# Performance work log

Measured on AMD Instinct MI355X. Metric: run time of the kernel, lower is better.

## Reference

```python
import jax, jax.numpy as jnp
import numpy as np

N = 100000   # nodes
E = 1600000  # edges (node pairs)
D = 64       # msg_feature_len
H = 128      # hidden width of gate/message MLPs


def setup_inputs() -> dict:
    key = jax.random.key(0)
    ks = jax.random.split(key, 10)
    s = 0.05
    return {
        "node_weights": jax.random.uniform(ks[0], (N, 1), dtype=jnp.float32),
        "node_prev_features": jax.random.normal(ks[1], (N, D), dtype=jnp.float32),
        "self_idx": jax.random.randint(ks[2], (E,), 0, N),
        "neighbor_idx": jax.random.randint(ks[3], (E,), 0, N),
        "gw1": jax.random.normal(ks[4], (2 * D, H), dtype=jnp.float32) * s,
        "gb1": jnp.zeros((H,), jnp.float32),
        "gw2": jax.random.normal(ks[5], (H, 1), dtype=jnp.float32) * s,
        "gb2": jnp.zeros((1,), jnp.float32),
        "mw1": jax.random.normal(ks[6], (2 * D, H), dtype=jnp.float32) * s,
        "mb1": jnp.zeros((H,), jnp.float32),
        "mw2": jax.random.normal(ks[7], (H, D), dtype=jnp.float32) * s,
        "mb2": jnp.zeros((D,), jnp.float32),
        "pow_p": jax.random.normal(ks[8], (1,), dtype=jnp.float32),
    }


def reference(node_weights, node_prev_features, self_idx, neighbor_idx,
              gw1, gb1, gw2, gb2, mw1, mb1, mw2, mb2, pow_p):
    # gather + concat: message [E, 2D]
    msg = jnp.concatenate(
        [node_prev_features[self_idx], node_prev_features[neighbor_idx]], axis=1)
    w = node_weights[neighbor_idx]  # [E, 1]

    # gate MLP (Linear -> ReLU -> Linear): [E, 1]
    gate = jax.nn.relu(msg @ gw1 + gb1) @ gw2 + gb2
    # segment-softmax over edges grouped by self_idx, weighted by w**pow
    gmax = jax.ops.segment_max(gate, self_idx, num_segments=N)  # [N, 1]
    gate = (w ** pow_p) * jnp.exp(gate - gmax[self_idx])
    gsum = jax.ops.segment_sum(gate, self_idx, num_segments=N)  # [N, 1]
    gate = gate / (gsum[self_idx] + 1e-10)

    # message MLP: [E, D]
    x = jax.nn.relu(msg @ mw1 + mb1) @ mw2 + mb2

    # weighted scatter-sum back to nodes; single head -> mean is identity
    node_update = jax.ops.segment_sum(gate * x, self_idx, num_segments=N)
    return node_update + node_prev_features
```

## Files before the change

### kernel.cpp

```cpp
#include <hip/hip_runtime.h>
#include <hip/hip_bf16.h>

typedef __bf16 bf16x8 __attribute__((ext_vector_type(8)));
typedef float f32x4 __attribute__((ext_vector_type(4)));

#define WIN 64
#define TILE 112
#define CHUNK 7
#define LSTR 136
#define SCAN_BLK 1024
#define SENT 0x7f7f7f7f

__global__ void k_wconv(const float* __restrict__ gw1, const float* __restrict__ mw1,
                        const float* __restrict__ mw2,
                        __bf16* __restrict__ Bt, __bf16* __restrict__ mw2t,
                        int* __restrict__ hist, int* __restrict__ s_lo,
                        int* __restrict__ s_hi, int N, int NB)
{
    int i = blockIdx.x * 256 + threadIdx.x;
    if (i < 32768) {
        int c = i >> 6, k = i & 63;
        float v;
        if (c < 128)      v = gw1[k * 128 + c];
        else if (c < 256) v = gw1[(64 + k) * 128 + (c - 128)];
        else if (c < 384) v = mw1[k * 128 + (c - 256)];
        else              v = mw1[(64 + k) * 128 + (c - 384)];
        Bt[i] = (__bf16)v;
    } else if (i < 40960) {
        int j = i - 32768;
        int c = j >> 7, k = j & 127;
        mw2t[j] = (__bf16)mw2[k * 64 + c];
    }
    if (i < N) hist[i] = 0;
    if (i < NB) { s_lo[i] = SENT; s_hi[i] = 0; }
}

__global__ void __launch_bounds__(256, 4)
k_tab(const float* __restrict__ feat, const __bf16* __restrict__ Bt,
      const float* __restrict__ gb1, const float* __restrict__ mb1,
      const int* __restrict__ selfi, int* __restrict__ hist,
      __bf16* __restrict__ Tp, __bf16* __restrict__ Tq, int N, int E)
{
    for (int e = blockIdx.x * 256 + threadIdx.x; e < E; e += gridDim.x * 256)
        atomicAdd(&hist[selfi[e]], 1);

    const int tid = threadIdx.x;
    const int lane = tid & 63, wv = tid >> 6;
    const int la = lane & 15, kg = lane >> 4;
    const int r0 = blockIdx.x * 16;
    if (r0 >= N) return;

    bf16x8 a[2];
    #pragma unroll
    for (int kk = 0; kk < 2; ++kk) {
        const int rr = min(r0 + la, N - 1);
        const float* src = feat + (size_t)rr * 64 + kk * 32 + kg * 8;
        f32x4 f0 = *reinterpret_cast<const f32x4*>(src);
        f32x4 f1 = *reinterpret_cast<const f32x4*>(src + 4);
        #pragma unroll
        for (int j = 0; j < 4; ++j) { a[kk][j] = (__bf16)f0[j]; a[kk][4 + j] = (__bf16)f1[j]; }
    }
    #pragma unroll
    for (int j = 0; j < 8; ++j) {
        const int c = wv * 128 + j * 16 + la;
        float bias = 0.f;
        if (c < 128) bias = gb1[c];
        else if (c >= 256 && c < 384) bias = mb1[c - 256];
        f32x4 acc = {bias, bias, bias, bias};
        #pragma unroll
        for (int kk = 0; kk < 2; ++kk) {
            bf16x8 bb = *reinterpret_cast<const bf16x8*>(Bt + (size_t)c * 64 + kk * 32 + kg * 8);
            acc = __builtin_amdgcn_mfma_f32_16x16x32_bf16(a[kk], bb, acc, 0, 0, 0);
        }
        #pragma unroll
        for (int i = 0; i < 4; ++i) {
            const int row = r0 + kg * 4 + i;
            if (row < N) {
                const __bf16 v = (__bf16)acc[i];
                if (c < 128)      Tp[(size_t)row * 256 + c] = v;
                else if (c < 256) Tq[(size_t)row * 256 + (c - 128)] = v;
                else if (c < 384) Tp[(size_t)row * 256 + 128 + (c - 256)] = v;
                else              Tq[(size_t)row * 256 + 128 + (c - 384)] = v;
            }
        }
    }
}

__global__ void k_scan1(const int* __restrict__ hist, int* __restrict__ incl,
                        int* __restrict__ bsum, int N)
{
    __shared__ int sd[SCAN_BLK];
    int i = blockIdx.x * SCAN_BLK + threadIdx.x;
    int v = (i < N) ? hist[i] : 0;
    sd[threadIdx.x] = v;
    __syncthreads();
    for (int off = 1; off < SCAN_BLK; off <<= 1) {
        int t = (threadIdx.x >= off) ? sd[threadIdx.x - off] : 0;
        __syncthreads();
        sd[threadIdx.x] += t;
        __syncthreads();
    }
    if (i < N) incl[i] = sd[threadIdx.x];
    if (threadIdx.x == SCAN_BLK - 1) bsum[blockIdx.x] = sd[SCAN_BLK - 1];
}

__global__ void k_scanb(const int* __restrict__ bsum, int* __restrict__ boff, int nb)
{
    __shared__ int sd[256];
    const int t = threadIdx.x;
    int v = (t < nb) ? bsum[t] : 0;
    sd[t] = v;
    __syncthreads();
    for (int off = 1; off < 256; off <<= 1) {
        int u = (t >= off) ? sd[t - off] : 0;
        __syncthreads();
        sd[t] += u;
        __syncthreads();
    }
    if (t < nb) boff[t] = sd[t] - v;
}

__global__ void k_scan23(const int* __restrict__ incl, const int* __restrict__ hist,
                         const int* __restrict__ boff,
                         int* __restrict__ cursor, int* __restrict__ starts,
                         int* __restrict__ s_lo, int* __restrict__ s_hi,
                         float* __restrict__ wp, const float* __restrict__ nodew,
                         const float* __restrict__ powp,
                         const float* __restrict__ prev, float* __restrict__ out,
                         int N, int E)
{
    int i = blockIdx.x * SCAN_BLK + threadIdx.x;
    if (i >= N) return;
    const int h = hist[i];
    const int v = incl[i] - h + boff[blockIdx.x];
    cursor[i] = v;
    starts[i] = v;
    wp[i] = __powf(nodew[i], powp[0]);
    if (h > 0) {
        const int b = v / WIN;
        atomicMin(&s_lo[b], i);
        atomicMax(&s_hi[b], i + 1);
    } else {
        const float* ps = prev + (size_t)i * 64;
        float* po = out + (size_t)i * 64;
        for (int k = 0; k < 64; ++k) po[k] = ps[k];
    }
}

__global__ void k_scatter(const int* __restrict__ selfi, const int* __restrict__ nbri,
                          int* __restrict__ cursor, int* __restrict__ nbr_p, int E)
{
    int e = blockIdx.x * 256 + threadIdx.x;
    if (e >= E) return;
    int s = selfi[e];
    int pos = atomicAdd(&cursor[s], 1);
    nbr_p[pos] = nbri[e];
}

__global__ void __launch_bounds__(256, 4)
k_fused(const __bf16* __restrict__ Tp, const __bf16* __restrict__ Tq,
        const int* __restrict__ nbr_p, const int* __restrict__ starts,
        const int* __restrict__ s_lo, const int* __restrict__ s_hi,
        const float* __restrict__ wp,
        const float* __restrict__ gw2, const float* __restrict__ gb2,
        const __bf16* __restrict__ mw2t, const float* __restrict__ mb2,
        const float* __restrict__ prev, float* __restrict__ out,
        int N, int E)
{
    __shared__ __align__(16) __bf16 hlds[TILE][LSTR];
    __shared__ float logit_s[TILE];
    __shared__ float nbrw_s[TILE];
    __shared__ float ginv_s[WIN];
    __shared__ int st_s[WIN + 1];

    const int b = blockIdx.x;
    const int s0 = s_lo[b];
    if (s0 == SENT) return;
    const int s1 = s_hi[b];
    const int nseg = s1 - s0;
    const int e0 = starts[s0];
    const int e1 = (s1 < N) ? starts[s1] : E;
    int ne = e1 - e0;
    if (ne > TILE) ne = TILE;

    const int tid = threadIdx.x;
    for (int i = tid; i < ne; i += 256)
        nbrw_s[i] = wp[nbr_p[e0 + i]];
    for (int j = tid; j <= nseg; j += 256)
        st_s[j] = (j < nseg) ? starts[s0 + j] : e1;
    __syncthreads();

    const int lane = tid & 63, wv = tid >> 6;
    const int g16 = tid >> 4, il = tid & 15;

    {
        const float b2v = gb2[0];
        float w2f[8];
        {
            f32x4 wa = *reinterpret_cast<const f32x4*>(gw2 + il * 8);
            f32x4 wb = *reinterpret_cast<const f32x4*>(gw2 + il * 8 + 4);
            w2f[0] = wa[0]; w2f[1] = wa[1]; w2f[2] = wa[2]; w2f[3] = wa[3];
            w2f[4] = wb[0]; w2f[5] = wb[1]; w2f[6] = wb[2]; w2f[7] = wb[3];
        }
        const int ck = (ne + 15) >> 4;
        const int rb = g16 * ck;
        const int re = min(rb + ck, ne);
        if (rb < re) {
            bf16x8 qg[CHUNK], qm[CHUNK];
            #pragma unroll
            for (int j = 0; j < CHUNK; ++j) {
                if (rb + j < re) {
                    const int nn = nbr_p[e0 + rb + j];
                    const __bf16* tq = Tq + (size_t)nn * 256 + il * 8;
                    qg[j] = *reinterpret_cast<const bf16x8*>(tq);
                    qm[j] = *reinterpret_cast<const bf16x8*>(tq + 128);
                }
            }
            int cur;
            {
                int lo = 0, hi = nseg - 1;
                while (lo < hi) {
                    const int mid = (lo + hi + 1) >> 1;
                    if (st_s[mid] <= e0 + rb) lo = mid; else hi = mid - 1;
                }
                cur = lo;
            }
            int curlim = st_s[cur + 1];
            float pgf[8], pmf[8];
            {
                const __bf16* tp = Tp + (size_t)(s0 + cur) * 256 + il * 8;
                bf16x8 pg = *reinterpret_cast<const bf16x8*>(tp);
                bf16x8 pm = *reinterpret_cast<const bf16x8*>(tp + 128);
                #pragma unroll
                for (int j = 0; j < 8; ++j) { pgf[j] = (float)pg[j]; pmf[j] = (float)pm[j]; }
            }
            #pragma unroll
            for (int j = 0; j < CHUNK; ++j) {
                if (rb + j < re) {
                    const int r = rb + j;
                    if (e0 + r >= curlim) {
                        do { ++cur; curlim = st_s[cur + 1]; } while (e0 + r >= curlim);
                        const __bf16* tp = Tp + (size_t)(s0 + cur) * 256 + il * 8;
                        bf16x8 pg = *reinterpret_cast<const bf16x8*>(tp);
                        bf16x8 pm = *reinterpret_cast<const bf16x8*>(tp + 128);
                        #pragma unroll
                        for (int q = 0; q < 8; ++q) { pgf[q] = (float)pg[q]; pmf[q] = (float)pm[q]; }
                    }
                    float lg = 0.f;
                    bf16x8 hv;
                    #pragma unroll
                    for (int q = 0; q < 8; ++q) {
                        lg = fmaf(fmaxf(pgf[q] + (float)qg[j][q], 0.f), w2f[q], lg);
                        hv[q] = (__bf16)fmaxf(pmf[q] + (float)qm[j][q], 0.f);
                    }
                    *reinterpret_cast<bf16x8*>(&hlds[r][il * 8]) = hv;
                    #pragma unroll
                    for (int sh = 1; sh < 16; sh <<= 1)
                        lg += __shfl_xor(lg, sh, 16);
                    if (il == 0) logit_s[r] = lg + b2v;
                }
            }
        }
    }
    __syncthreads();

    const int la = lane & 15, kg = lane >> 4;
    const int row0[2] = {wv * 16, 64 + wv * 16};
    const bool lv[2] = {row0[0] < ne, (wv < 3) && (row0[1] < ne)};

    f32x4 c2[2][4] = {};
    #pragma unroll
    for (int kk = 0; kk < 4; ++kk) {
        const int kbase = kk * 32 + kg * 8;
        bf16x8 a[2];
        #pragma unroll
        for (int m = 0; m < 2; ++m)
            if (lv[m]) a[m] = *reinterpret_cast<const bf16x8*>(&hlds[row0[m] + la][kbase]);
        #pragma unroll
        for (int n = 0; n < 4; ++n) {
            bf16x8 bb = *reinterpret_cast<const bf16x8*>(mw2t + (size_t)(n * 16 + la) * 128 + kbase);
            #pragma unroll
            for (int m = 0; m < 2; ++m)
                if (lv[m]) c2[m][n] = __builtin_amdgcn_mfma_f32_16x16x32_bf16(a[m], bb, c2[m][n], 0, 0, 0);
        }
    }

    for (int j = g16; j < nseg; j += 16) {
        int a0 = st_s[j] - e0;
        int a1 = st_s[j + 1] - e0;
        if (a1 > ne) a1 = ne;
        float mx = -3.4e38f;
        for (int idx = a0 + il; idx < a1; idx += 16)
            mx = fmaxf(mx, logit_s[idx]);
        #pragma unroll
        for (int sh = 1; sh < 16; sh <<= 1)
            mx = fmaxf(mx, __shfl_xor(mx, sh, 16));
        float sum = 0.f;
        for (int idx = a0 + il; idx < a1; idx += 16) {
            const float g = nbrw_s[idx] * __expf(logit_s[idx] - mx);
            logit_s[idx] = g;
            sum += g;
        }
        #pragma unroll
        for (int sh = 1; sh < 16; sh <<= 1)
            sum += __shfl_xor(sum, sh, 16);
        if (il == 0) ginv_s[j] = 1.f / (sum + 1e-10f);
    }
    __syncthreads();

    float (*xb)[68] = reinterpret_cast<float(*)[68]>(&hlds[0][0]);
    #pragma unroll
    for (int m = 0; m < 2; ++m) {
        if (!lv[m]) continue;
        float cf[4];
        #pragma unroll
        for (int i = 0; i < 4; ++i) {
            const int row = row0[m] + kg * 4 + i;
            cf[i] = (row < ne) ? logit_s[row] : 0.f;
        }
        #pragma unroll
        for (int n = 0; n < 4; ++n) {
            const float b2v = mb2[n * 16 + la];
            #pragma unroll
            for (int i = 0; i < 4; ++i)
                xb[row0[m] + kg * 4 + i][n * 16 + la] = cf[i] * (c2[m][n][i] + b2v);
        }
    }
    __syncthreads();

    for (int j = wv; j < nseg; j += 4) {
        int a0 = st_s[j] - e0;
        int a1 = st_s[j + 1] - e0;
        if (a1 > ne) a1 = ne;
        if (a1 <= a0) continue;
        float sum = 0.f;
        for (int r = a0; r < a1; ++r) sum += xb[r][lane];
        const float gi = ginv_s[j];
        const size_t o = (size_t)(s0 + j) * 64 + lane;
        out[o] = prev[o] + sum * gi;
    }
}

extern "C" void kernel_launch(void* const* d_in, const int* in_sizes, int n_in,
                              void* d_out, int out_size, void* d_ws, size_t ws_size,
                              hipStream_t stream)
{
    const float* node_w = (const float*)d_in[0];
    const float* prev   = (const float*)d_in[1];
    const int*   selfi  = (const int*)d_in[2];
    const int*   nbri   = (const int*)d_in[3];
    const float* gw1 = (const float*)d_in[4];
    const float* gb1 = (const float*)d_in[5];
    const float* gw2 = (const float*)d_in[6];
    const float* gb2 = (const float*)d_in[7];
    const float* mw1 = (const float*)d_in[8];
    const float* mb1 = (const float*)d_in[9];
    const float* mw2 = (const float*)d_in[10];
    const float* mb2 = (const float*)d_in[11];
    const float* powp = (const float*)d_in[12];
    const int N = in_sizes[0];
    const int E = in_sizes[2];
    float* out = (float*)d_out;
    const int NB = (E + WIN - 1) / WIN;

    char* ws = (char*)d_ws;
    size_t off = 0;
    auto alloc = [&](size_t bytes) {
        void* p = ws + off;
        off = (off + bytes + 255) & ~(size_t)255;
        return p;
    };
    __bf16* Tp     = (__bf16*)alloc((size_t)N * 256 * 2);
    __bf16* Tq     = (__bf16*)alloc((size_t)N * 256 * 2);
    __bf16* Bt     = (__bf16*)alloc(512 * 64 * 2);
    __bf16* mw2t   = (__bf16*)alloc(64 * 128 * 2);
    int* nbr_p     = (int*)alloc((size_t)E * 4);
    int* hist      = (int*)alloc((size_t)N * 4);
    int* cursor    = (int*)alloc((size_t)N * 4);
    int* starts    = (int*)alloc((size_t)N * 4);
    int* incl      = (int*)alloc((size_t)N * 4);
    float* wp      = (float*)alloc((size_t)N * 4);
    int* s_lo      = (int*)alloc((size_t)NB * 4);
    int* s_hi      = (int*)alloc((size_t)NB * 4);
    const int nb = (N + SCAN_BLK - 1) / SCAN_BLK;
    int* bsum      = (int*)alloc((size_t)nb * 4);
    int* boff      = (int*)alloc((size_t)nb * 4);

    int initN = N;
    if (initN < 40960) initN = 40960;
    if (initN < NB) initN = NB;
    k_wconv<<<(initN + 255) / 256, 256, 0, stream>>>(gw1, mw1, mw2, Bt, mw2t,
                                                     hist, s_lo, s_hi, N, NB);
    k_tab<<<(N + 15) / 16, 256, 0, stream>>>(prev, Bt, gb1, mb1, selfi, hist, Tp, Tq, N, E);
    k_scan1<<<nb, SCAN_BLK, 0, stream>>>(hist, incl, bsum, N);
    k_scanb<<<1, 256, 0, stream>>>(bsum, boff, nb);
    k_scan23<<<nb, SCAN_BLK, 0, stream>>>(incl, hist, boff, cursor, starts, s_lo, s_hi,
                                          wp, node_w, powp, prev, out, N, E);
    k_scatter<<<(E + 255) / 256, 256, 0, stream>>>(selfi, nbri, cursor, nbr_p, E);
    k_fused<<<NB, 256, 0, stream>>>(Tp, Tq, nbr_p, starts, s_lo, s_hi, wp,
                                    gw2, gb2, mw2t, mb2, prev, out, N, E);
}
```

Measured before the change: 574.7 us.

## Store neighbor-side hidden table in FP8 and fold node weight into logit

The neighbor-side projection table Tq is now stored as FP8 (e4m3) instead of bf16, with the gate and message halves interleaved in 16-byte groups. Each edge then gathers one 16-byte load instead of two. The per-node weight w**p becomes p*log(w), which is added to the logit before the softmax exponent; this drops the separate nbrw shared-memory staging and its extra gather pass. Occupancy on the fused kernel is raised to 5 blocks per SM. This halves random-gather bandwidth at the cost of FP8 precision on the neighbor activations, and log(0) becomes -inf if a weight is zero.

```diff
diff --git a/kernel.cpp b/kernel.cpp
--- a/kernel.cpp
+++ b/kernel.cpp
@@ -3,6 +3,7 @@
 
 typedef __bf16 bf16x8 __attribute__((ext_vector_type(8)));
 typedef float f32x4 __attribute__((ext_vector_type(4)));
+typedef float f32x2 __attribute__((ext_vector_type(2)));
 
 #define WIN 64
 #define TILE 112
@@ -39,7 +40,7 @@
 k_tab(const float* __restrict__ feat, const __bf16* __restrict__ Bt,
       const float* __restrict__ gb1, const float* __restrict__ mb1,
       const int* __restrict__ selfi, int* __restrict__ hist,
-      __bf16* __restrict__ Tp, __bf16* __restrict__ Tq, int N, int E)
+      __bf16* __restrict__ Tp, unsigned char* __restrict__ Tq, int N, int E)
 {
     for (int e = blockIdx.x * 256 + threadIdx.x; e < E; e += gridDim.x * 256)
         atomicAdd(&hist[selfi[e]], 1);
@@ -76,11 +77,19 @@
         for (int i = 0; i < 4; ++i) {
             const int row = r0 + kg * 4 + i;
             if (row < N) {
-                const __bf16 v = (__bf16)acc[i];
-                if (c < 128)      Tp[(size_t)row * 256 + c] = v;
-                else if (c < 256) Tq[(size_t)row * 256 + (c - 128)] = v;
-                else if (c < 384) Tp[(size_t)row * 256 + 128 + (c - 256)] = v;
-                else              Tq[(size_t)row * 256 + 128 + (c - 384)] = v;
+                if (c < 128) {
+                    Tp[(size_t)row * 256 + c] = (__bf16)acc[i];
+                } else if (c < 256) {
+                    const int qc = c - 128;
+                    const int pk = __builtin_amdgcn_cvt_pk_fp8_f32(acc[i], acc[i], 0, false);
+                    Tq[(size_t)row * 256 + (qc >> 3) * 16 + (qc & 7)] = (unsigned char)(pk & 0xff);
+                } else if (c < 384) {
+                    Tp[(size_t)row * 256 + 128 + (c - 256)] = (__bf16)acc[i];
+                } else {
+                    const int qc = c - 384;
+                    const int pk = __builtin_amdgcn_cvt_pk_fp8_f32(acc[i], acc[i], 0, false);
+                    Tq[(size_t)row * 256 + (qc >> 3) * 16 + 8 + (qc & 7)] = (unsigned char)(pk & 0xff);
+                }
             }
         }
     }
@@ -124,7 +133,7 @@
                          const int* __restrict__ boff,
                          int* __restrict__ cursor, int* __restrict__ starts,
                          int* __restrict__ s_lo, int* __restrict__ s_hi,
-                         float* __restrict__ wp, const float* __restrict__ nodew,
+                         float* __restrict__ lpw, const float* __restrict__ nodew,
                          const float* __restrict__ powp,
                          const float* __restrict__ prev, float* __restrict__ out,
                          int N, int E)
@@ -135,7 +144,7 @@
     const int v = incl[i] - h + boff[blockIdx.x];
     cursor[i] = v;
     starts[i] = v;
-    wp[i] = __powf(nodew[i], powp[0]);
+    lpw[i] = powp[0] * __logf(nodew[i]);
     if (h > 0) {
         const int b = v / WIN;
         atomicMin(&s_lo[b], i);
@@ -157,11 +166,11 @@
     nbr_p[pos] = nbri[e];
 }
 
-__global__ void __launch_bounds__(256, 4)
-k_fused(const __bf16* __restrict__ Tp, const __bf16* __restrict__ Tq,
+__global__ void __launch_bounds__(256, 5)
+k_fused(const __bf16* __restrict__ Tp, const unsigned char* __restrict__ Tq,
         const int* __restrict__ nbr_p, const int* __restrict__ starts,
         const int* __restrict__ s_lo, const int* __restrict__ s_hi,
-        const float* __restrict__ wp,
+        const float* __restrict__ lpw,
         const float* __restrict__ gw2, const float* __restrict__ gb2,
         const __bf16* __restrict__ mw2t, const float* __restrict__ mb2,
         const float* __restrict__ prev, float* __restrict__ out,
@@ -169,7 +178,6 @@
 {
     __shared__ __align__(16) __bf16 hlds[TILE][LSTR];
     __shared__ float logit_s[TILE];
-    __shared__ float nbrw_s[TILE];
     __shared__ float ginv_s[WIN];
     __shared__ int st_s[WIN + 1];
 
@@ -184,8 +192,6 @@
     if (ne > TILE) ne = TILE;
 
     const int tid = threadIdx.x;
-    for (int i = tid; i < ne; i += 256)
-        nbrw_s[i] = wp[nbr_p[e0 + i]];
     for (int j = tid; j <= nseg; j += 256)
         st_s[j] = (j < nseg) ? starts[s0 + j] : e1;
     __syncthreads();
@@ -206,14 +212,14 @@
         const int rb = g16 * ck;
         const int re = min(rb + ck, ne);
         if (rb < re) {
-            bf16x8 qg[CHUNK], qm[CHUNK];
+            uint4 qv[CHUNK];
+            float lpv[CHUNK];
             #pragma unroll
             for (int j = 0; j < CHUNK; ++j) {
                 if (rb + j < re) {
                     const int nn = nbr_p[e0 + rb + j];
-                    const __bf16* tq = Tq + (size_t)nn * 256 + il * 8;
-                    qg[j] = *reinterpret_cast<const bf16x8*>(tq);
-                    qm[j] = *reinterpret_cast<const bf16x8*>(tq + 128);
+                    qv[j] = *reinterpret_cast<const uint4*>(Tq + (size_t)nn * 256 + il * 16);
+                    lpv[j] = lpw[nn];
                 }
             }
             int cur;
@@ -246,18 +252,28 @@
                         #pragma unroll
                         for (int q = 0; q < 8; ++q) { pgf[q] = (float)pg[q]; pmf[q] = (float)pm[q]; }
                     }
+                    f32x2 g01 = __builtin_amdgcn_cvt_pk_f32_fp8(qv[j].x, false);
+                    f32x2 g23 = __builtin_amdgcn_cvt_pk_f32_fp8(qv[j].x, true);
+                    f32x2 g45 = __builtin_amdgcn_cvt_pk_f32_fp8(qv[j].y, false);
+                    f32x2 g67 = __builtin_amdgcn_cvt_pk_f32_fp8(qv[j].y, true);
+                    f32x2 m01 = __builtin_amdgcn_cvt_pk_f32_fp8(qv[j].z, false);
+                    f32x2 m23 = __builtin_amdgcn_cvt_pk_f32_fp8(qv[j].z, true);
+                    f32x2 m45 = __builtin_amdgcn_cvt_pk_f32_fp8(qv[j].w, false);
+                    f32x2 m67 = __builtin_amdgcn_cvt_pk_f32_fp8(qv[j].w, true);
+                    float qgv[8] = {g01[0], g01[1], g23[0], g23[1], g45[0], g45[1], g67[0], g67[1]};
+                    float qmv[8] = {m01[0], m01[1], m23[0], m23[1], m45[0], m45[1], m67[0], m67[1]};
                     float lg = 0.f;
                     bf16x8 hv;
                     #pragma unroll
                     for (int q = 0; q < 8; ++q) {
-                        lg = fmaf(fmaxf(pgf[q] + (float)qg[j][q], 0.f), w2f[q], lg);
-                        hv[q] = (__bf16)fmaxf(pmf[q] + (float)qm[j][q], 0.f);
+                        lg = fmaf(fmaxf(pgf[q] + qgv[q], 0.f), w2f[q], lg);
+                        hv[q] = (__bf16)fmaxf(pmf[q] + qmv[q], 0.f);
                     }
                     *reinterpret_cast<bf16x8*>(&hlds[r][il * 8]) = hv;
                     #pragma unroll
                     for (int sh = 1; sh < 16; sh <<= 1)
                         lg += __shfl_xor(lg, sh, 16);
-                    if (il == 0) logit_s[r] = lg + b2v;
+                    if (il == 0) logit_s[r] = lg + b2v + lpv[j];
                 }
             }
         }
@@ -297,7 +313,7 @@
             mx = fmaxf(mx, __shfl_xor(mx, sh, 16));
         float sum = 0.f;
         for (int idx = a0 + il; idx < a1; idx += 16) {
-            const float g = nbrw_s[idx] * __expf(logit_s[idx] - mx);
+            const float g = __expf(logit_s[idx] - mx);
             logit_s[idx] = g;
             sum += g;
         }
@@ -370,21 +386,21 @@
         off = (off + bytes + 255) & ~(size_t)255;
         return p;
     };
-    __bf16* Tp     = (__bf16*)alloc((size_t)N * 256 * 2);
-    __bf16* Tq     = (__bf16*)alloc((size_t)N * 256 * 2);
-    __bf16* Bt     = (__bf16*)alloc(512 * 64 * 2);
-    __bf16* mw2t   = (__bf16*)alloc(64 * 128 * 2);
-    int* nbr_p     = (int*)alloc((size_t)E * 4);
-    int* hist      = (int*)alloc((size_t)N * 4);
-    int* cursor    = (int*)alloc((size_t)N * 4);
-    int* starts    = (int*)alloc((size_t)N * 4);
-    int* incl      = (int*)alloc((size_t)N * 4);
-    float* wp      = (float*)alloc((size_t)N * 4);
-    int* s_lo      = (int*)alloc((size_t)NB * 4);
-    int* s_hi      = (int*)alloc((size_t)NB * 4);
+    __bf16* Tp           = (__bf16*)alloc((size_t)N * 256 * 2);
+    unsigned char* Tq    = (unsigned char*)alloc((size_t)N * 256);
+    __bf16* Bt           = (__bf16*)alloc(512 * 64 * 2);
+    __bf16* mw2t         = (__bf16*)alloc(64 * 128 * 2);
+    int* nbr_p           = (int*)alloc((size_t)E * 4);
+    int* hist            = (int*)alloc((size_t)N * 4);
+    int* cursor          = (int*)alloc((size_t)N * 4);
+    int* starts          = (int*)alloc((size_t)N * 4);
+    int* incl            = (int*)alloc((size_t)N * 4);
+    float* lpw           = (float*)alloc((size_t)N * 4);
+    int* s_lo            = (int*)alloc((size_t)NB * 4);
+    int* s_hi            = (int*)alloc((size_t)NB * 4);
     const int nb = (N + SCAN_BLK - 1) / SCAN_BLK;
-    int* bsum      = (int*)alloc((size_t)nb * 4);
-    int* boff      = (int*)alloc((size_t)nb * 4);
+    int* bsum            = (int*)alloc((size_t)nb * 4);
+    int* boff            = (int*)alloc((size_t)nb * 4);
 
     int initN = N;
     if (initN < 40960) initN = 40960;
@@ -395,8 +411,8 @@
     k_scan1<<<nb, SCAN_BLK, 0, stream>>>(hist, incl, bsum, N);
     k_scanb<<<1, 256, 0, stream>>>(bsum, boff, nb);
     k_scan23<<<nb, SCAN_BLK, 0, stream>>>(incl, hist, boff, cursor, starts, s_lo, s_hi,
-                                          wp, node_w, powp, prev, out, N, E);
+                                          lpw, node_w, powp, prev, out, N, E);
     k_scatter<<<(E + 255) / 256, 256, 0, stream>>>(selfi, nbri, cursor, nbr_p, E);
-    k_fused<<<NB, 256, 0, stream>>>(Tp, Tq, nbr_p, starts, s_lo, s_hi, wp,
+    k_fused<<<NB, 256, 0, stream>>>(Tp, Tq, nbr_p, starts, s_lo, s_hi, lpw,
                                     gw2, gb2, mw2t, mb2, prev, out, N, E);
 }
```

Result: faster. 504.9 us (-12.2%).
